# Performance work log

Hardware: AMD Instinct MI355X
Metric: run time of the kernel (lower is better)

Reference implementation:

```python
import jax, jax.numpy as jnp
import numpy as np

NUM_EMBEDDINGS = 1024
EMBEDDING_DIM = 64
COMMITMENT_COST = 0.25


def setup_inputs() -> dict:
    key = jax.random.key(0)
    k1, k2 = jax.random.split(key)
    inputs = jax.random.normal(k1, (8, 128, 128, EMBEDDING_DIM), dtype=jnp.float32)
    # nn.Embedding init: uniform(-1/K, 1/K)
    codebook = jax.random.uniform(
        k2, (NUM_EMBEDDINGS, EMBEDDING_DIM), dtype=jnp.float32,
        minval=-1.0 / NUM_EMBEDDINGS, maxval=1.0 / NUM_EMBEDDINGS)
    return {"inputs": inputs, "codebook": codebook}


def reference(inputs, codebook):
    input_shape = inputs.shape
    flat = inputs.reshape(-1, EMBEDDING_DIM)  # [N, D]
    distances = (jnp.sum(flat * flat, axis=1, keepdims=True)
                 + jnp.sum(codebook * codebook, axis=1)
                 - 2.0 * jnp.matmul(flat, codebook.T))  # [N, K]
    encoding_indices = jnp.argmin(distances, axis=1)  # [N]
    # one-hot @ codebook == direct gather
    quantized = codebook[encoding_indices].reshape(input_shape)
    e_latent_loss = jnp.mean((jax.lax.stop_gradient(quantized) - inputs) ** 2)
    q_latent_loss = jnp.mean((quantized - jax.lax.stop_gradient(inputs)) ** 2)
    vq_loss = q_latent_loss + COMMITMENT_COST * e_latent_loss
    # straight-through estimator
    quantized = inputs + jax.lax.stop_gradient(quantized - inputs)
    return (quantized, vq_loss, encoding_indices[:, None])
```

## Files before the change

### kernel.cpp

```cpp
#include <hip/hip_runtime.h>


typedef _Float16 f16x8 __attribute__((ext_vector_type(8)));
typedef _Float16 f16x4 __attribute__((ext_vector_type(4)));
typedef float f32x4 __attribute__((ext_vector_type(4)));

constexpr int Dm = 64;
constexpr int Kn = 1024;
constexpr long NR = 131072;
constexpr long QE = NR * (long)Dm;
constexpr int RB = 64;
constexpr int NBLK = (int)(NR / RB);
constexpr int CH = 64;
constexpr int NCH = Kn / CH;
constexpr int SP4 = 17;

constexpr size_t SE_OFF   = 0;
constexpr size_t CBH_OFF  = 4096;
constexpr size_t CNT_OFF  = CBH_OFF + 131072;
constexpr size_t HARD_OFF = CNT_OFF + 256;
constexpr size_t PART_OFF = HARD_OFF + 4 * 131072;
constexpr size_t WS_REQ   = PART_OFF + 16384;

__global__ __launch_bounds__(256) void vq_prep(const float* __restrict__ cb,
                                               float* __restrict__ se,
                                               _Float16* __restrict__ cbh,
                                               int* __restrict__ cnt)
{
    int j = blockIdx.x * 256 + threadIdx.x;
    const float* e = cb + (size_t)j * Dm;
    _Float16* h = cbh + (size_t)j * Dm;
    float s = 0.f;
    #pragma unroll
    for (int d = 0; d < Dm; ++d) s = fmaf(e[d], e[d], s);
    se[j] = s;
    #pragma unroll
    for (int d = 0; d < Dm; ++d) h[d] = (_Float16)(e[d] * 1024.0f);
    if (j == 0) *cnt = 0;
}

__global__ __launch_bounds__(256, 4) void vq_pass1(
    const float* __restrict__ inp, const _Float16* __restrict__ cbh,
    const float* __restrict__ seg, float* __restrict__ out,
    int* __restrict__ hard_list, int* __restrict__ cnt)
{
    __shared__ __align__(16) _Float16 xh[RB * 72];
    __shared__ float gq[RB][17];
    __shared__ float wm1[4][RB], wm2[4][RB];
    __shared__ int   wi1[4][RB];

    const int tid = threadIdx.x;
    const long rbase = (long)blockIdx.x * RB;

    {
        const float4* src = reinterpret_cast<const float4*>(inp + rbase * Dm);
        #pragma unroll
        for (int r = 0; r < 4; ++r) {
            int g = r * 256 + tid;
            int row = g >> 4, col = g & 15;
            float4 v = src[g];
            f16x4 h = { (_Float16)v.x, (_Float16)v.y, (_Float16)v.z, (_Float16)v.w };
            *reinterpret_cast<f16x4*>(xh + row * 72 + col * 4) = h;
            gq[row][col] = fabsf(v.x) + fabsf(v.y) + fabsf(v.z) + fabsf(v.w);
        }
    }
    __syncthreads();

    const int w = tid >> 6, l = tid & 63;
    const int arow = l & 15, kg = l >> 4;

    f16x8 a0[4], a1[4];
    #pragma unroll
    for (int rt = 0; rt < 4; ++rt) {
        const _Float16* ap = xh + (rt * 16 + arow) * 72 + kg * 8;
        a0[rt] = *reinterpret_cast<const f16x8*>(ap);
        a1[rt] = *reinterpret_cast<const f16x8*>(ap + 32);
    }

    float mn1[4][4], mn2[4][4]; int ix1[4][4];
    #pragma unroll
    for (int rt = 0; rt < 4; ++rt)
        #pragma unroll
        for (int r = 0; r < 4; ++r) {
            mn1[rt][r] = __builtin_inff(); mn2[rt][r] = __builtin_inff();
            ix1[rt][r] = 0;
        }

    const int code0 = w * 256 + arow;
    const _Float16* bp = cbh + (size_t)code0 * Dm + kg * 8;

    #pragma unroll 4
    for (int t = 0; t < 16; ++t) {
        const _Float16* tp = bp + t * 16 * Dm;
        f16x8 b0 = *reinterpret_cast<const f16x8*>(tp);
        f16x8 b1 = *reinterpret_cast<const f16x8*>(tp + 32);
        const int code = code0 + t * 16;
        const float sec = seg[code];
        #pragma unroll
        for (int rt = 0; rt < 4; ++rt) {
            f32x4 acc = {0.f, 0.f, 0.f, 0.f};
            acc = __builtin_amdgcn_mfma_f32_16x16x32_f16(a0[rt], b0, acc, 0, 0, 0);
            acc = __builtin_amdgcn_mfma_f32_16x16x32_f16(a1[rt], b1, acc, 0, 0, 0);
            #pragma unroll
            for (int r = 0; r < 4; ++r) {
                float m = fmaf(acc[r], -0.001953125f, sec);
                float m2n;
                asm("v_med3_f32 %0, %1, %2, %3"
                    : "=v"(m2n) : "v"(m), "v"(mn1[rt][r]), "v"(mn2[rt][r]));
                mn2[rt][r] = m2n;
                ix1[rt][r] = (m < mn1[rt][r]) ? code : ix1[rt][r];
                mn1[rt][r] = fminf(mn1[rt][r], m);
            }
        }
    }

    #pragma unroll
    for (int rt = 0; rt < 4; ++rt)
        #pragma unroll
        for (int r = 0; r < 4; ++r) {
            float m1v = mn1[rt][r], m2v = mn2[rt][r]; int i1v = ix1[rt][r];
            #pragma unroll
            for (int off = 1; off < 16; off <<= 1) {
                float om1 = __shfl_xor(m1v, off);
                float om2 = __shfl_xor(m2v, off);
                int   oi1 = __shfl_xor(i1v, off);
                float mx  = fmaxf(m1v, om1);
                float nm2;
                asm("v_min3_f32 %0, %1, %2, %3"
                    : "=v"(nm2) : "v"(m2v), "v"(om2), "v"(mx));
                i1v = (om1 < m1v) ? oi1 : i1v;
                m1v = fminf(m1v, om1);
                m2v = nm2;
            }
            if (arow == 0) {
                const int row = rt * 16 + kg * 4 + r;
                wm1[w][row] = m1v; wm2[w][row] = m2v; wi1[w][row] = i1v;
            }
        }
    __syncthreads();

    if (tid < RB) {
        float m1v = wm1[0][tid], m2v = wm2[0][tid]; int i1v = wi1[0][tid];
        #pragma unroll
        for (int q = 1; q < 4; ++q) {
            float am1 = wm1[q][tid], am2 = wm2[q][tid]; int ai = wi1[q][tid];
            float mx  = fmaxf(m1v, am1);
            float nm2;
            asm("v_min3_f32 %0, %1, %2, %3"
                : "=v"(nm2) : "v"(m2v), "v"(am2), "v"(mx));
            i1v = (am1 < m1v) ? ai : i1v;
            m1v = fminf(m1v, am1);
            m2v = nm2;
        }
        float gg = gq[tid][0];
        #pragma unroll
        for (int c = 1; c < 16; ++c) gg += gq[tid][c];
        const float T = fmaf(gg, 5.2e-6f, 4.0e-5f);
        const int easy = (m2v - m1v) > T;
        if (easy) out[QE + 1 + rbase + tid] = (float)i1v;
        unsigned long long hm = __ballot(!easy);
        const int nh = __popcll(hm);
        int base = 0;
        if (tid == 0 && nh) base = atomicAdd(cnt, nh);
        base = __shfl(base, 0);
        if (!easy) {
            const int pos = base + __popcll(hm & ((1ull << tid) - 1ull));
            hard_list[pos] = (int)(rbase + tid);
        }
    }
}

__global__ __launch_bounds__(256) void vq_pass2(
    const float* __restrict__ inp, const float* __restrict__ cb,
    const float* __restrict__ seg, float* __restrict__ out,
    const int* __restrict__ hard_list, const int* __restrict__ cnt)
{
    __shared__ float4 xs[RB * SP4];
    __shared__ float4 es[CH * SP4];
    __shared__ float  ses[Kn];
    __shared__ float  sxs[RB];
    __shared__ int    hr[RB];
    __shared__ float  bd[RB * 17];
    __shared__ int    bi[RB * 17];

    const int tid = threadIdx.x;
    const int tr = tid & 15;
    const int tc = tid >> 4;

    #pragma unroll
    for (int k = 0; k < 4; ++k) ses[tid + 256 * k] = seg[tid + 256 * k];

    const int total = *cnt;
    const int nchunk = (total + RB - 1) / RB;
    const float4* gcb = reinterpret_cast<const float4*>(cb);

    for (int c = blockIdx.x; c < nchunk; c += gridDim.x) {
        __syncthreads();
        if (tid < RB) {
            int gi = c * RB + tid;
            hr[tid] = (gi < total) ? hard_list[gi] : -1;
        }
        __syncthreads();

        #pragma unroll
        for (int r = 0; r < 4; ++r) {
            int g = r * 256 + tid;
            int row = g >> 4, col = g & 15;
            int gr = hr[row];
            float4 v = {0.f, 0.f, 0.f, 0.f};
            if (gr >= 0)
                v = *reinterpret_cast<const float4*>(inp + (size_t)gr * Dm + col * 4);
            xs[row * SP4 + col] = v;
        }
        __syncthreads();

        if (tid < RB) {
            const float* xr = reinterpret_cast<const float*>(&xs[tid * SP4]);
            float s = 0.f;
            #pragma unroll
            for (int d = 0; d < Dm; ++d) s = fmaf(xr[d], xr[d], s);
            sxs[tid] = s;
        }
        __syncthreads();

        float sxr[4];
        #pragma unroll
        for (int rr = 0; rr < 4; ++rr) sxr[rr] = sxs[tr + 16 * rr];

        float best[4]; int bidx[4];
        #pragma unroll
        for (int rr = 0; rr < 4; ++rr) { best[rr] = __builtin_inff(); bidx[rr] = 0; }

        for (int ch = 0; ch < NCH; ++ch) {
            __syncthreads();
            #pragma unroll
            for (int r = 0; r < 4; ++r) {
                int g = r * 256 + tid;
                es[(g >> 4) * SP4 + (g & 15)] = gcb[(size_t)ch * (CH * Dm / 4) + g];
            }
            __syncthreads();

            float acc[4][4];
            #pragma unroll
            for (int rr = 0; rr < 4; ++rr)
                #pragma unroll
                for (int cc = 0; cc < 4; ++cc) acc[rr][cc] = 0.f;

            #pragma unroll 4
            for (int db = 0; db < 16; ++db) {
                float4 xf[4], ef[4];
                #pragma unroll
                for (int rr = 0; rr < 4; ++rr) xf[rr] = xs[(tr + 16 * rr) * SP4 + db];
                #pragma unroll
                for (int cc = 0; cc < 4; ++cc) ef[cc] = es[(tc + 16 * cc) * SP4 + db];
                #pragma unroll
                for (int rr = 0; rr < 4; ++rr)
                    #pragma unroll
                    for (int cc = 0; cc < 4; ++cc) {
                        float a = acc[rr][cc];
                        a = fmaf(xf[rr].x, ef[cc].x, a);
                        a = fmaf(xf[rr].y, ef[cc].y, a);
                        a = fmaf(xf[rr].z, ef[cc].z, a);
                        a = fmaf(xf[rr].w, ef[cc].w, a);
                        acc[rr][cc] = a;
                    }
            }

            const int cbase = ch * CH;
            #pragma unroll
            for (int cc = 0; cc < 4; ++cc) {
                const int code = cbase + tc + 16 * cc;
                const float sec = ses[code];
                #pragma unroll
                for (int rr = 0; rr < 4; ++rr) {
                    float dist = (sxr[rr] + sec) - 2.0f * acc[rr][cc];
                    if (dist < best[rr]) { best[rr] = dist; bidx[rr] = code; }
                }
            }
        }

        #pragma unroll
        for (int rr = 0; rr < 4; ++rr) {
            int row = tr + 16 * rr;
            bd[row * 17 + tc] = best[rr];
            bi[row * 17 + tc] = bidx[rr];
        }
        __syncthreads();

        if (tid < RB && hr[tid] >= 0) {
            float b = bd[tid * 17]; int ii = bi[tid * 17];
            #pragma unroll
            for (int q = 1; q < 16; ++q) {
                float d = bd[tid * 17 + q]; int iq = bi[tid * 17 + q];
                if (d < b || (d == b && iq < ii)) { b = d; ii = iq; }
            }
            out[QE + 1 + hr[tid]] = (float)ii;
        }
    }
}

__global__ __launch_bounds__(256) void vq_quant(const float* __restrict__ inp,
                                                const float* __restrict__ cb,
                                                float* __restrict__ out,
                                                double* __restrict__ part)
{
    __shared__ double red[256];
    const int tid = threadIdx.x;
    const long rbase = (long)blockIdx.x * RB;
    const int r2 = tid >> 2;
    const int dq = (tid & 3) * 16;
    const long grow = rbase + r2;

    const int code = (int)out[QE + 1 + grow];
    const float* xr2 = inp + grow * (long)Dm + dq;
    const float* q2  = cb + (size_t)code * Dm + dq;
    float* outq = out + grow * (long)Dm + dq;
    double s = 0.0;
    #pragma unroll
    for (int d0 = 0; d0 < 16; d0 += 4) {
        float4 xv = *reinterpret_cast<const float4*>(xr2 + d0);
        float4 qv = *reinterpret_cast<const float4*>(q2 + d0);
        float4 ov;
        float m0 = qv.x - xv.x; ov.x = xv.x + m0;
        float m1 = qv.y - xv.y; ov.y = xv.y + m1;
        float m2 = qv.z - xv.z; ov.z = xv.z + m2;
        float m3 = qv.w - xv.w; ov.w = xv.w + m3;
        s += (double)m0*m0 + (double)m1*m1 + (double)m2*m2 + (double)m3*m3;
        *reinterpret_cast<float4*>(outq + d0) = ov;
    }

    red[tid] = s;
    __syncthreads();
    for (int k = 128; k > 0; k >>= 1) {
        if (tid < k) red[tid] += red[tid + k];
        __syncthreads();
    }
    if (tid == 0) part[blockIdx.x] = red[0];
}

__global__ __launch_bounds__(256) void vq_fin(const double* __restrict__ part,
                                              float* __restrict__ out)
{
    __shared__ double red[256];
    const int tid = threadIdx.x;
    double s = 0.0;
    #pragma unroll
    for (int k = 0; k < 8; ++k) s += part[tid + 256 * k];
    red[tid] = s;
    __syncthreads();
    for (int k = 128; k > 0; k >>= 1) {
        if (tid < k) red[tid] += red[tid + k];
        __syncthreads();
    }
    if (tid == 0) {
        float m = (float)(red[0] / (double)QE);
        out[QE] = m + 0.25f * m;
    }
}

extern "C" void kernel_launch(void* const* d_in, const int* in_sizes, int n_in,
                              void* d_out, int out_size, void* d_ws, size_t ws_size,
                              hipStream_t stream)
{
    const float* inp = (const float*)d_in[0];
    const float* cb  = (const float*)d_in[1];
    float* out = (float*)d_out;
    char* ws = (char*)d_ws;

    float*    se   = (float*)(ws + SE_OFF);
    _Float16* cbh  = (_Float16*)(ws + CBH_OFF);
    int*      cnt  = (int*)(ws + CNT_OFF);
    int*      hard = (int*)(ws + HARD_OFF);
    double*   part = (double*)(ws + PART_OFF);

    vq_prep<<<4, 256, 0, stream>>>(cb, se, cbh, cnt);
    vq_pass1<<<NBLK, 256, 0, stream>>>(inp, cbh, se, out, hard, cnt);
    vq_pass2<<<1024, 256, 0, stream>>>(inp, cb, se, out, hard, cnt);
    vq_quant<<<NBLK, 256, 0, stream>>>(inp, cb, out, part);
    vq_fin<<<1, 256, 0, stream>>>(part, out);
}
```

Before: 169.3 us.

## Stage codebook norms in LDS, restructure input load, drop inline asm

The pass-1 kernel now copies all 1024 codebook squared norms into shared memory and reads them from there instead of from global memory inside the main loop. The input tile load changes to one thread per quarter-row with scalar fp16 stores. A separate 64-thread loop re-reads each row from global memory to compute the abs-sum threshold, replacing the per-chunk partial sums. Several other changes come along: the inline v_med3/v_min3 asm is replaced with fminf/fmaxf expressions, the main loop unroll drops from 4 to 2, and pass2's grid is halved. These trade extra global re-reads and a serial 64-element loop in a few threads for less LDS and simpler code.

Result: faster. 145.7 us (-13.9%).

```diff
diff --git a/kernel.cpp b/kernel.cpp
--- a/kernel.cpp
+++ b/kernel.cpp
@@ -2,7 +2,6 @@
 
 
 typedef _Float16 f16x8 __attribute__((ext_vector_type(8)));
-typedef _Float16 f16x4 __attribute__((ext_vector_type(4)));
 typedef float f32x4 __attribute__((ext_vector_type(4)));
 
 constexpr int Dm = 64;
@@ -45,24 +44,34 @@
     int* __restrict__ hard_list, int* __restrict__ cnt)
 {
     __shared__ __align__(16) _Float16 xh[RB * 72];
-    __shared__ float gq[RB][17];
+    __shared__ float se[Kn];
+    __shared__ float gs[RB];
     __shared__ float wm1[4][RB], wm2[4][RB];
     __shared__ int   wi1[4][RB];
 
     const int tid = threadIdx.x;
     const long rbase = (long)blockIdx.x * RB;
 
+    #pragma unroll
+    for (int k = 0; k < 4; ++k) se[tid + 256 * k] = seg[tid + 256 * k];
+
     {
-        const float4* src = reinterpret_cast<const float4*>(inp + rbase * Dm);
-        #pragma unroll
-        for (int r = 0; r < 4; ++r) {
-            int g = r * 256 + tid;
-            int row = g >> 4, col = g & 15;
-            float4 v = src[g];
-            f16x4 h = { (_Float16)v.x, (_Float16)v.y, (_Float16)v.z, (_Float16)v.w };
-            *reinterpret_cast<f16x4*>(xh + row * 72 + col * 4) = h;
-            gq[row][col] = fabsf(v.x) + fabsf(v.y) + fabsf(v.z) + fabsf(v.w);
-        }
+        const int r = tid >> 2, q = tid & 3;
+        const float* src = inp + (rbase + r) * Dm + q * 16;
+        _Float16* dst = xh + r * 72 + q * 16;
+        #pragma unroll
+        for (int i = 0; i < 4; ++i) {
+            float4 v = *reinterpret_cast<const float4*>(src + 4 * i);
+            dst[4*i+0] = (_Float16)v.x; dst[4*i+1] = (_Float16)v.y;
+            dst[4*i+2] = (_Float16)v.z; dst[4*i+3] = (_Float16)v.w;
+        }
+    }
+    if (tid < RB) {
+        const float* xr = inp + (rbase + tid) * Dm;
+        float g = 0.f;
+        #pragma unroll
+        for (int d = 0; d < Dm; ++d) g += fabsf(xr[d]);
+        gs[tid] = g;
     }
     __syncthreads();
 
@@ -89,13 +98,13 @@
     const int code0 = w * 256 + arow;
     const _Float16* bp = cbh + (size_t)code0 * Dm + kg * 8;
 
-    #pragma unroll 4
+    #pragma unroll 2
     for (int t = 0; t < 16; ++t) {
         const _Float16* tp = bp + t * 16 * Dm;
         f16x8 b0 = *reinterpret_cast<const f16x8*>(tp);
         f16x8 b1 = *reinterpret_cast<const f16x8*>(tp + 32);
         const int code = code0 + t * 16;
-        const float sec = seg[code];
+        const float sec = se[code];
         #pragma unroll
         for (int rt = 0; rt < 4; ++rt) {
             f32x4 acc = {0.f, 0.f, 0.f, 0.f};
@@ -104,10 +113,7 @@
             #pragma unroll
             for (int r = 0; r < 4; ++r) {
                 float m = fmaf(acc[r], -0.001953125f, sec);
-                float m2n;
-                asm("v_med3_f32 %0, %1, %2, %3"
-                    : "=v"(m2n) : "v"(m), "v"(mn1[rt][r]), "v"(mn2[rt][r]));
-                mn2[rt][r] = m2n;
+                mn2[rt][r] = fminf(mn2[rt][r], fmaxf(mn1[rt][r], m));
                 ix1[rt][r] = (m < mn1[rt][r]) ? code : ix1[rt][r];
                 mn1[rt][r] = fminf(mn1[rt][r], m);
             }
@@ -124,10 +130,7 @@
                 float om1 = __shfl_xor(m1v, off);
                 float om2 = __shfl_xor(m2v, off);
                 int   oi1 = __shfl_xor(i1v, off);
-                float mx  = fmaxf(m1v, om1);
-                float nm2;
-                asm("v_min3_f32 %0, %1, %2, %3"
-                    : "=v"(nm2) : "v"(m2v), "v"(om2), "v"(mx));
+                float nm2 = fminf(fminf(m2v, om2), fmaxf(m1v, om1));
                 i1v = (om1 < m1v) ? oi1 : i1v;
                 m1v = fminf(m1v, om1);
                 m2v = nm2;
@@ -144,18 +147,12 @@
         #pragma unroll
         for (int q = 1; q < 4; ++q) {
             float am1 = wm1[q][tid], am2 = wm2[q][tid]; int ai = wi1[q][tid];
-            float mx  = fmaxf(m1v, am1);
-            float nm2;
-            asm("v_min3_f32 %0, %1, %2, %3"
-                : "=v"(nm2) : "v"(m2v), "v"(am2), "v"(mx));
+            float nm2 = fminf(fminf(m2v, am2), fmaxf(m1v, am1));
             i1v = (am1 < m1v) ? ai : i1v;
             m1v = fminf(m1v, am1);
             m2v = nm2;
         }
-        float gg = gq[tid][0];
-        #pragma unroll
-        for (int c = 1; c < 16; ++c) gg += gq[tid][c];
-        const float T = fmaf(gg, 5.2e-6f, 4.0e-5f);
+        const float T = fmaf(gs[tid], 5.2e-6f, 4.0e-5f);
         const int easy = (m2v - m1v) > T;
         if (easy) out[QE + 1 + rbase + tid] = (float)i1v;
         unsigned long long hm = __ballot(!easy);
@@ -375,7 +372,7 @@
 
     vq_prep<<<4, 256, 0, stream>>>(cb, se, cbh, cnt);
     vq_pass1<<<NBLK, 256, 0, stream>>>(inp, cbh, se, out, hard, cnt);
-    vq_pass2<<<1024, 256, 0, stream>>>(inp, cb, se, out, hard, cnt);
+    vq_pass2<<<512, 256, 0, stream>>>(inp, cb, se, out, hard, cnt);
     vq_quant<<<NBLK, 256, 0, stream>>>(inp, cb, out, part);
     vq_fin<<<1, 256, 0, stream>>>(part, out);
 }
```
